# Kernel optimization log

Hardware: AMD Instinct MI355X
Metric: run time of the kernel (lower is better)

The kernel has to match this reference:

```python
import jax, jax.numpy as jnp
import numpy as np

B, S, HID = 2, 2048, 2048
H, KV, D = 16, 4, 128
ROT = 64           # partial rotary dim (= cos.shape[-1])
EMB = 128          # router embedding dim
TAU, BASE = 0.4, 3.0
EPS = 1e-6


def rotate_half(x):
    h = x.shape[-1] // 2
    return jnp.concatenate([-x[..., h:], x[..., :h]], axis=-1)


def rmsnorm(x, w, eps=EPS):
    # Qwen3.5: zero-init weight, (1 + w) scaling, compute in fp32
    xf = x.astype(jnp.float32)
    o = xf * jax.lax.rsqrt(jnp.mean(xf * xf, axis=-1, keepdims=True) + eps)
    return (o * (1.0 + w.astype(jnp.float32))).astype(x.dtype)


def _rope_tables():
    inv_freq = 1.0 / (10000.0 ** (np.arange(0, ROT, 2, dtype=np.float32) / ROT))
    t = np.arange(S, dtype=np.float32)
    freqs = np.outer(t, inv_freq)                 # [S, ROT/2]
    emb = np.concatenate([freqs, freqs], axis=-1)  # [S, ROT]
    cos = np.broadcast_to(np.cos(emb), (B, S, ROT)).copy()
    sin = np.broadcast_to(np.sin(emb), (B, S, ROT)).copy()
    return jnp.asarray(cos), jnp.asarray(sin)


def setup_inputs() -> dict:
    key = jax.random.key(0)
    ks = jax.random.split(key, 10)
    sc = 0.02
    cos, sin = _rope_tables()
    return {
        "hidden_states": jax.random.normal(ks[0], (B, S, HID), jnp.float32),
        "cos": cos,
        "sin": sin,
        # projection weights stored as [in, out] (torch Linear weight transposed)
        "Wq": jax.random.normal(ks[1], (HID, H * D * 2), jnp.float32) * sc,
        "Wk": jax.random.normal(ks[2], (HID, KV * D), jnp.float32) * sc,
        "Wv": jax.random.normal(ks[3], (HID, KV * D), jnp.float32) * sc,
        "Wo": jax.random.normal(ks[4], (H * D, HID), jnp.float32) * sc,
        "q_norm_w": jnp.zeros((D,), jnp.float32),
        "k_norm_w": jnp.zeros((D,), jnp.float32),
        "Wr": jax.random.normal(ks[5], (HID, EMB), jnp.float32) * sc,   # router linear
        "Wd": jax.random.normal(ks[6], (EMB, D), jnp.float32) * sc,     # router decoder
        "ln_g": jnp.ones((EMB,), jnp.float32),
        "ln_b": jnp.zeros((EMB,), jnp.float32),
        "rnn_state": jnp.zeros((EMB,), jnp.float32),
    }


def _forward(hidden_states, cos, sin, Wq, Wk, Wv, Wo, q_norm_w, k_norm_w,
             Wr, Wd, ln_g, ln_b, rnn_state):
    b, s, _ = hidden_states.shape
    # doubled q_proj -> query + gate
    qkv = jnp.einsum('bsh,hd->bsd', hidden_states, Wq).reshape(b, s, H, 2 * D)
    q, gate = qkv[..., :D], qkv[..., D:]
    gate = gate.reshape(b, s, H * D)
    k = jnp.einsum('bsh,hd->bsd', hidden_states, Wk).reshape(b, s, KV, D)
    v = jnp.einsum('bsh,hd->bsd', hidden_states, Wv).reshape(b, s, KV, D)
    # per-head RMSNorm then [b, h, s, d]
    q = rmsnorm(q, q_norm_w).transpose(0, 2, 1, 3)
    k = rmsnorm(k, k_norm_w).transpose(0, 2, 1, 3)
    v = v.transpose(0, 2, 1, 3)

    # --- head-dim router (gumbel-sigmoid, straight-through hard round) ---
    emb = jnp.einsum('bsh,he->bse', hidden_states, Wr) + rnn_state
    mu = jnp.mean(emb, -1, keepdims=True)
    var = jnp.mean((emb - mu) ** 2, -1, keepdims=True)
    ln = (emb - mu) * jax.lax.rsqrt(var + 1e-5) * ln_g + ln_b
    logits = jnp.einsum('bse,ed->bsd', jax.nn.gelu(ln, approximate=False), Wd)
    gum = -jnp.log(jax.random.exponential(jax.random.key(42), logits.shape, jnp.float32))
    y_soft = jax.nn.sigmoid((logits + gum + BASE) / TAU)
    binary = jax.lax.stop_gradient(jnp.round(y_soft) - y_soft) + y_soft  # [b, s, D]
    mask = binary[:, None, :, :]  # broadcast over heads: [b, 1, s, D]

    q = q * mask
    k = k * mask

    # partial RoPE on first ROT dims (qk_index=None training path)
    c = cos[:, None, :, :]
    si = sin[:, None, :, :]
    def rope(x):
        xr, xp = x[..., :ROT], x[..., ROT:]
        return jnp.concatenate([xr * c + rotate_half(xr) * si, xp], axis=-1)
    q = rope(q)
    k = rope(k)

    # GQA: repeat kv heads
    rep = H // KV
    k = jnp.repeat(k, rep, axis=1)
    v = jnp.repeat(v, rep, axis=1)

    scores = jnp.einsum('bhqd,bhkd->bhqk', q, k) / np.sqrt(D).astype(np.float32)
    causal = jnp.tril(jnp.ones((s, s), bool))
    scores = jnp.where(causal, scores, jnp.finfo(jnp.float32).min)
    attn = jax.nn.softmax(scores.astype(jnp.float32), axis=-1).astype(q.dtype)
    out = jnp.einsum('bhqk,bhkd->bhqd', attn, v)
    out = out.transpose(0, 2, 1, 3).reshape(b, s, H * D)
    out = out * jax.nn.sigmoid(gate)   # output gate
    return jnp.einsum('bsd,dh->bsh', out, Wo)


def reference(hidden_states, cos, sin, Wq, Wk, Wv, Wo, q_norm_w, k_norm_w,
              Wr, Wd, ln_g, ln_b, rnn_state):
    return _forward(hidden_states, cos, sin, Wq, Wk, Wv, Wo, q_norm_w, k_norm_w,
                    Wr, Wd, ln_g, ln_b, rnn_state)
```

## Files before the change

### kernel.cpp

```cpp
#include <hip/hip_runtime.h>
#include <math.h>

typedef __bf16 bf16;
typedef bf16 bf16x8 __attribute__((ext_vector_type(8)));
typedef bf16 bf16x4 __attribute__((ext_vector_type(4)));
typedef float f32x4 __attribute__((ext_vector_type(4)));

#define BB 2
#define SS 2048
#define HIDN 2048
#define NH 16
#define NKV 4
#define DD 128
#define NROT 64
#define NPROJ 5248

__device__ __forceinline__ float waveAllReduceSum(float v) {
#pragma unroll
  for (int o = 1; o < 64; o <<= 1) v += __shfl_xor(v, o, 64);
  return v;
}

__device__ __forceinline__ int xcd_swz(int orig, int nwg) {
  return (orig & 7) * (nwg >> 3) + (orig >> 3);
}

__device__ __forceinline__ void gload16(const bf16* g, bf16* l) {
  __builtin_amdgcn_global_load_lds((const __attribute__((address_space(1))) void*)g,
                                   (__attribute__((address_space(3))) void*)l, 16, 0, 0);
}

__device__ __forceinline__ void do_transpose(bf16 (*tile)[72], const float* __restrict__ W,
                                             bf16* __restrict__ WT, int K, int N, int rowOff,
                                             int bx, int by, int t) {
  int n0 = bx * 64, k0 = by * 64;
  {
    int c4 = (t & 15) * 4, r = t >> 4;
#pragma unroll
    for (int p = 0; p < 4; p++) {
      int row = p * 16 + r;
      float4 v = *reinterpret_cast<const float4*>(W + (size_t)(k0 + row) * N + n0 + c4);
      bf16x4 o = {(bf16)v.x, (bf16)v.y, (bf16)v.z, (bf16)v.w};
      *reinterpret_cast<bf16x4*>(&tile[row][c4]) = o;
    }
  }
  __syncthreads();
  {
    int ln = t & 7, n = t >> 3;
#pragma unroll
    for (int p = 0; p < 2; p++) {
      int nn = p * 32 + n;
      bf16x8 o;
#pragma unroll
      for (int j = 0; j < 8; j++) o[j] = tile[ln * 8 + j][nn];
      *reinterpret_cast<bf16x8*>(WT + (size_t)(rowOff + n0 + nn) * K + k0 + ln * 8) = o;
    }
  }
  __syncthreads();
}

__global__ __launch_bounds__(256) void prep_weights(const float* __restrict__ hidden,
                                                    const float* __restrict__ Wq,
                                                    const float* __restrict__ Wk,
                                                    const float* __restrict__ Wv,
                                                    const float* __restrict__ Wr,
                                                    const float* __restrict__ Wo,
                                                    bf16* __restrict__ hb,
                                                    bf16* __restrict__ WTall,
                                                    bf16* __restrict__ WoT) {
  __shared__ bf16 tile[64][72];
  int id = blockIdx.x, t = threadIdx.x;
  if (id < 4096) {
    int i = (id * 256 + t) * 8;
    float4 v0 = *reinterpret_cast<const float4*>(hidden + i);
    float4 v1 = *reinterpret_cast<const float4*>(hidden + i + 4);
    bf16x8 o = {(bf16)v0.x, (bf16)v0.y, (bf16)v0.z, (bf16)v0.w,
                (bf16)v1.x, (bf16)v1.y, (bf16)v1.z, (bf16)v1.w};
    *reinterpret_cast<bf16x8*>(hb + i) = o;
    return;
  }
  int id2 = id - 4096;
  if (id2 < 2048) { do_transpose(tile, Wq, WTall, 2048, 4096, 0, id2 & 63, id2 >> 6, t); return; }
  id2 -= 2048;
  if (id2 < 256) { do_transpose(tile, Wk, WTall, 2048, 512, 4096, id2 & 7, id2 >> 3, t); return; }
  id2 -= 256;
  if (id2 < 256) { do_transpose(tile, Wv, WTall, 2048, 512, 4608, id2 & 7, id2 >> 3, t); return; }
  id2 -= 256;
  if (id2 < 64) { do_transpose(tile, Wr, WTall, 2048, 128, 5120, id2 & 1, id2 >> 1, t); return; }
  id2 -= 64;
  do_transpose(tile, Wo, WoT, 2048, 2048, 0, id2 & 31, id2 >> 5, t);
}

template <typename CT>
__global__ __launch_bounds__(256) void gemm_bt(const bf16* __restrict__ A,
                                               const bf16* __restrict__ Bt,
                                               CT* __restrict__ C, int M, int N, int K) {
  __shared__ bf16 lA[128 * 64];
  __shared__ bf16 lB[128 * 64];
  const int nbx = N >> 7;
  int wg = xcd_swz(blockIdx.x, gridDim.x);
  int bx = wg % nbx, by = wg / nbx;
  const int t = threadIdx.x;
  const int l = t & 63, w = t >> 6;
  const int wr = w >> 1, wc = w & 1;
  const int lr = l & 15, lhi = l >> 4;

  f32x4 acc[4][4];
#pragma unroll
  for (int m = 0; m < 4; m++)
#pragma unroll
    for (int n = 0; n < 4; n++) acc[m][n] = f32x4{0.f, 0.f, 0.f, 0.f};

  const int rowA0 = by * 128, rowB0 = bx * 128;
  const int nkt = K >> 6;
  for (int kt = 0; kt < nkt; ++kt) {
    __syncthreads();
#pragma unroll
    for (int it = 0; it < 4; ++it) {
      int slot = it * 256 + t;
      int row = slot >> 3, sl = slot & 7;
      gload16(A + (size_t)(rowA0 + row) * K + kt * 64 + ((sl ^ (row & 7)) << 3), lA + slot * 8);
      gload16(Bt + (size_t)(rowB0 + row) * K + kt * 64 + ((sl ^ (row & 7)) << 3), lB + slot * 8);
    }
    __syncthreads();
#pragma unroll
    for (int kc = 0; kc < 2; ++kc) {
      bf16x8 af[4], bg[4];
#pragma unroll
      for (int m = 0; m < 4; m++) {
        int row = wr * 64 + m * 16 + lr;
        af[m] = *reinterpret_cast<const bf16x8*>((char*)lA + row * 128 + (((kc * 4 + lhi) ^ (row & 7)) << 4));
      }
#pragma unroll
      for (int n = 0; n < 4; n++) {
        int row = wc * 64 + n * 16 + lr;
        bg[n] = *reinterpret_cast<const bf16x8*>((char*)lB + row * 128 + (((kc * 4 + lhi) ^ (row & 7)) << 4));
      }
      __builtin_amdgcn_s_setprio(1);
#pragma unroll
      for (int m = 0; m < 4; m++)
#pragma unroll
        for (int n = 0; n < 4; n++)
          acc[m][n] = __builtin_amdgcn_mfma_f32_16x16x32_bf16(af[m], bg[n], acc[m][n], 0, 0, 0);
      __builtin_amdgcn_s_setprio(0);
    }
  }
#pragma unroll
  for (int m = 0; m < 4; m++)
#pragma unroll
    for (int n = 0; n < 4; n++)
#pragma unroll
      for (int r = 0; r < 4; r++) {
        int grow = rowA0 + wr * 64 + m * 16 + lhi * 4 + r;
        int gcol = rowB0 + wc * 64 + n * 16 + lr;
        C[(size_t)grow * N + gcol] = (CT)acc[m][n][r];
      }
}

__device__ __forceinline__ unsigned rotl32(unsigned x, int r) { return (x << r) | (x >> (32 - r)); }

__device__ __forceinline__ float gumbel42(unsigned i) {
  const unsigned half = (unsigned)(BB * SS * DD) / 2u;
  unsigned x0, x1;
  int word;
  if (i < half) { x0 = i; x1 = i + half; word = 0; }
  else          { x0 = i - half; x1 = i; word = 1; }
  const unsigned k0 = 0u, k1 = 42u;
  const unsigned k2 = k0 ^ k1 ^ 0x1BD11BDAu;
  x0 += k0; x1 += k1;
#define TF_R(r) { x0 += x1; x1 = rotl32(x1, r); x1 ^= x0; }
  TF_R(13) TF_R(15) TF_R(26) TF_R(6)
  x0 += k1; x1 += k2 + 1u;
  TF_R(17) TF_R(29) TF_R(16) TF_R(24)
  x0 += k2; x1 += k0 + 2u;
  TF_R(13) TF_R(15) TF_R(26) TF_R(6)
  x0 += k0; x1 += k1 + 3u;
  TF_R(17) TF_R(29) TF_R(16) TF_R(24)
  x0 += k1; x1 += k2 + 4u;
  TF_R(13) TF_R(15) TF_R(26) TF_R(6)
  x0 += k2; x1 += k0 + 5u;
#undef TF_R
  unsigned bits = word ? x1 : x0;
  float u = __uint_as_float((bits >> 9) | 0x3f800000u) - 1.0f;
  float ex = -log1pf(-u);
  return -logf(ex);
}

__global__ __launch_bounds__(128) void mask_kernel(const bf16* __restrict__ qkva,
                                                   const float* __restrict__ rnn,
                                                   const float* __restrict__ lng,
                                                   const float* __restrict__ lnb,
                                                   const float* __restrict__ Wd,
                                                   bf16* __restrict__ maskb) {
  int row = blockIdx.x;
  int t = threadIdx.x;
  int l = t & 63, w = t >> 6;
  __shared__ float redm[2], redv[2], gsh[128];
  float e = (float)qkva[(size_t)row * NPROJ + 5120 + t] + rnn[t];
  float s1 = waveAllReduceSum(e);
  if (l == 0) redm[w] = s1;
  __syncthreads();
  float mu = (redm[0] + redm[1]) * (1.0f / 128.0f);
  float dv = (e - mu) * (e - mu);
  float s2 = waveAllReduceSum(dv);
  if (l == 0) redv[w] = s2;
  __syncthreads();
  float var = (redv[0] + redv[1]) * (1.0f / 128.0f);
  float ln = (e - mu) * rsqrtf(var + 1e-5f) * lng[t] + lnb[t];
  float g = 0.5f * ln * (1.0f + erff(ln * 0.7071067811865475f));
  gsh[t] = g;
  __syncthreads();
  float logit = 0.f;
#pragma unroll 8
  for (int e2 = 0; e2 < 128; e2++) logit += gsh[e2] * Wd[e2 * 128 + t];
  float gum = gumbel42((unsigned)(row * 128 + t));
  float x = (logit + gum + 3.0f) * 2.5f;
  float y = 1.0f / (1.0f + expf(-x));
  maskb[(size_t)row * 128 + t] = (bf16)rintf(y);
}

#define QSCALE (0.08838834764831845f * 1.4426950408889634f)

__global__ __launch_bounds__(256) void qkv_prep(const bf16* __restrict__ qkva,
                                                const bf16* __restrict__ maskb,
                                                const float* __restrict__ qw,
                                                const float* __restrict__ kw,
                                                const float* __restrict__ cosT,
                                                const float* __restrict__ sinT,
                                                bf16* __restrict__ wq,
                                                bf16* __restrict__ sgate,
                                                bf16* __restrict__ wk,
                                                bf16* __restrict__ wvt) {
  int id = blockIdx.x, t = threadIdx.x;
  if (id < 4096) {
    int g = t >> 4, ln = t & 15;
    int hr = id * 16 + g;
    int h = hr & 15, row = hr >> 4;
    int b = row >> 11, s = row & 2047;
    const bf16* qp = qkva + (size_t)row * NPROJ + h * 256 + ln * 8;
    bf16x8 q8 = *reinterpret_cast<const bf16x8*>(qp);
    bf16x8 g8 = *reinterpret_cast<const bf16x8*>(qp + 128);
    bf16x8 m8 = *reinterpret_cast<const bf16x8*>(maskb + (size_t)row * 128 + ln * 8);
    float qf[8], ss = 0.f;
#pragma unroll
    for (int j = 0; j < 8; j++) { qf[j] = (float)q8[j]; ss += qf[j] * qf[j]; }
#pragma unroll
    for (int o = 1; o < 16; o <<= 1) ss += __shfl_xor(ss, o, 16);
    float rinv = rsqrtf(ss * (1.0f / 128.0f) + 1e-6f);
    alignas(16) float wv[8];
    const float4* qw4 = reinterpret_cast<const float4*>(qw);
    *reinterpret_cast<float4*>(&wv[0]) = qw4[ln * 2];
    *reinterpret_cast<float4*>(&wv[4]) = qw4[ln * 2 + 1];
    float qm[8];
#pragma unroll
    for (int j = 0; j < 8; j++) qm[j] = qf[j] * rinv * (1.0f + wv[j]) * (float)m8[j];
    alignas(16) float c8[8], s8[8];
    if (ln < 8) {
      const float4* c4 = reinterpret_cast<const float4*>(cosT + (size_t)row * 64);
      const float4* sn4 = reinterpret_cast<const float4*>(sinT + (size_t)row * 64);
      *reinterpret_cast<float4*>(&c8[0]) = c4[ln * 2];
      *reinterpret_cast<float4*>(&c8[4]) = c4[ln * 2 + 1];
      *reinterpret_cast<float4*>(&s8[0]) = sn4[ln * 2];
      *reinterpret_cast<float4*>(&s8[4]) = sn4[ln * 2 + 1];
    }
    float po[8];
#pragma unroll
    for (int j = 0; j < 8; j++) po[j] = __shfl_xor(qm[j], 4, 16);
    bf16x8 oq, og;
#pragma unroll
    for (int j = 0; j < 8; j++) {
      float ov;
      if (ln < 4) ov = qm[j] * c8[j] - po[j] * s8[j];
      else if (ln < 8) ov = qm[j] * c8[j] + po[j] * s8[j];
      else ov = qm[j];
      oq[j] = (bf16)(ov * QSCALE);
      og[j] = (bf16)(1.0f / (1.0f + expf(-(float)g8[j])));
    }
    size_t o = ((size_t)((b * 16 + h) * 2048 + s)) * 128 + ln * 8;
    *reinterpret_cast<bf16x8*>(wq + o) = oq;
    *reinterpret_cast<bf16x8*>(sgate + o) = og;
    return;
  }
  if (id < 5120) {
    int g = t >> 4, ln = t & 15;
    int hr = (id - 4096) * 16 + g;
    int kv = hr & 3, row = hr >> 2;
    int b = row >> 11, s = row & 2047;
    const bf16* kp = qkva + (size_t)row * NPROJ + 4096 + kv * 128 + ln * 8;
    bf16x8 k8 = *reinterpret_cast<const bf16x8*>(kp);
    bf16x8 m8 = *reinterpret_cast<const bf16x8*>(maskb + (size_t)row * 128 + ln * 8);
    float kf[8], ss = 0.f;
#pragma unroll
    for (int j = 0; j < 8; j++) { kf[j] = (float)k8[j]; ss += kf[j] * kf[j]; }
#pragma unroll
    for (int o = 1; o < 16; o <<= 1) ss += __shfl_xor(ss, o, 16);
    float rinv = rsqrtf(ss * (1.0f / 128.0f) + 1e-6f);
    alignas(16) float wv[8];
    const float4* kw4 = reinterpret_cast<const float4*>(kw);
    *reinterpret_cast<float4*>(&wv[0]) = kw4[ln * 2];
    *reinterpret_cast<float4*>(&wv[4]) = kw4[ln * 2 + 1];
    float km[8];
#pragma unroll
    for (int j = 0; j < 8; j++) km[j] = kf[j] * rinv * (1.0f + wv[j]) * (float)m8[j];
    alignas(16) float c8[8], s8[8];
    if (ln < 8) {
      const float4* c4 = reinterpret_cast<const float4*>(cosT + (size_t)row * 64);
      const float4* sn4 = reinterpret_cast<const float4*>(sinT + (size_t)row * 64);
      *reinterpret_cast<float4*>(&c8[0]) = c4[ln * 2];
      *reinterpret_cast<float4*>(&c8[4]) = c4[ln * 2 + 1];
      *reinterpret_cast<float4*>(&s8[0]) = sn4[ln * 2];
      *reinterpret_cast<float4*>(&s8[4]) = sn4[ln * 2 + 1];
    }
    float po[8];
#pragma unroll
    for (int j = 0; j < 8; j++) po[j] = __shfl_xor(km[j], 4, 16);
    bf16x8 ok;
#pragma unroll
    for (int j = 0; j < 8; j++) {
      float ov;
      if (ln < 4) ov = km[j] * c8[j] - po[j] * s8[j];
      else if (ln < 8) ov = km[j] * c8[j] + po[j] * s8[j];
      else ov = km[j];
      ok[j] = (bf16)ov;
    }
    *reinterpret_cast<bf16x8*>(wk + ((size_t)((b * 4 + kv) * 2048 + s)) * 128 + ln * 8) = ok;
    return;
  }
  {
    __shared__ bf16 tl[64][72];
    int vb = id - 5120;
    int dt = vb & 1;
    int st = (vb >> 1) & 31;
    int bkv = vb >> 6;
    int b = bkv >> 2, kv = bkv & 3;
    int tx = t & 63, ty = t >> 6;
    int s0 = st * 64, d0 = dt * 64;
#pragma unroll
    for (int i = 0; i < 16; i++) {
      int srow = ty + i * 4;
      tl[srow][tx] = qkva[(size_t)(b * 2048 + s0 + srow) * NPROJ + 4608 + kv * 128 + d0 + tx];
    }
    __syncthreads();
#pragma unroll
    for (int i = 0; i < 16; i++) {
      int drow = ty + i * 4;
      wvt[(size_t)((b * 4 + kv) * 128 + d0 + drow) * 2048 + s0 + tx] = tl[tx][drow];
    }
  }
}

__global__ __launch_bounds__(512) void attn_kernel(const bf16* __restrict__ wq,
                                                   const bf16* __restrict__ wk,
                                                   const bf16* __restrict__ wvt,
                                                   const bf16* __restrict__ sgate,
                                                   bf16* __restrict__ wattn) {
  __shared__ bf16 lK[2][64 * 128];
  __shared__ bf16 lV[2][128 * 64];
  __shared__ bf16 lP[8][16 * 64];
  int bid = blockIdx.x;
  int grp = bid & 7;
  int b = grp >> 2, kvh = grp & 3;
  int g32 = bid >> 3;
  int pp = g32 & 7;
  int h = kvh * 4 + (g32 >> 3);
  int bh = b * 16 + h;
  int t = threadIdx.x, l = t & 63, w = t >> 6;
  int lr = l & 15, lhi = l >> 4;

  const bf16* kbase = wk + (size_t)((b * 4 + kvh) * 2048) * 128;
  const bf16* vbase = wvt + (size_t)((b * 4 + kvh) * 128) * 2048;
  char* pb = (char*)(&lP[w][0]);

  const int n0 = 2 * pp + 2;

  auto stage = [&](int buf, int tt) {
#pragma unroll
    for (int it = 0; it < 2; ++it) {
      int slot = it * 512 + t;
      int row = slot >> 4, sl = slot & 15;
      gload16(kbase + (size_t)(tt * 64 + row) * 128 + ((sl ^ (row & 7)) << 3), lK[buf] + slot * 8);
      int row2 = slot >> 3, sl2 = slot & 7;
      gload16(vbase + (size_t)row2 * 2048 + tt * 64 + ((sl2 ^ (row2 & 7)) << 3), lV[buf] + slot * 8);
    }
  };

  bf16x8 aq[4];
  f32x4 oacc[8];
  float m_run, l_run;
  int qb128 = pp;

  auto load_q = [&](int qbv) {
    const bf16* qbase = wq + (size_t)(bh * 2048 + qbv * 128 + w * 16) * 128;
#pragma unroll
    for (int kc = 0; kc < 4; kc++)
      aq[kc] = *reinterpret_cast<const bf16x8*>(qbase + (size_t)lr * 128 + kc * 32 + lhi * 8);
  };
  load_q(pp);
#pragma unroll
  for (int db = 0; db < 8; db++) oacc[db] = f32x4{0.f, 0.f, 0.f, 0.f};
  m_run = -3.0e38f;
  l_run = 0.f;

  stage(0, 0);
  __syncthreads();
  int cur = 0;

  for (int i = 0; i < 34; ++i) {
    int tt = (i < n0) ? i : i - n0;
    if (i + 1 < 34) {
      int tn = (i + 1 < n0) ? (i + 1) : (i + 1 - n0);
      stage(cur ^ 1, tn);
    }
    int qrow0 = qb128 * 128 + w * 16;

    f32x4 sacc[4];
#pragma unroll
    for (int j = 0; j < 4; j++) sacc[j] = f32x4{0.f, 0.f, 0.f, 0.f};
    __builtin_amdgcn_s_setprio(1);
#pragma unroll
    for (int kc = 0; kc < 4; kc++)
#pragma unroll
      for (int j = 0; j < 4; j++) {
        int row = j * 16 + lr;
        bf16x8 ak = *reinterpret_cast<const bf16x8*>((char*)lK[cur] + row * 256 + (((kc * 4 + lhi) ^ (row & 7)) << 4));
        sacc[j] = __builtin_amdgcn_mfma_f32_16x16x32_bf16(ak, aq[kc], sacc[j], 0, 0, 0);
      }
    __builtin_amdgcn_s_setprio(0);

    if (tt * 64 + 63 > qrow0) {
      int qrow_g = qrow0 + lr;
#pragma unroll
      for (int j = 0; j < 4; j++)
#pragma unroll
        for (int r = 0; r < 4; r++) {
          int kg = tt * 64 + j * 16 + lhi * 4 + r;
          if (kg > qrow_g) sacc[j][r] = -1e30f;
        }
    }

    float m0 = fmaxf(fmaxf(sacc[0][0], sacc[0][1]), fmaxf(sacc[0][2], sacc[0][3]));
    float m1 = fmaxf(fmaxf(sacc[1][0], sacc[1][1]), fmaxf(sacc[1][2], sacc[1][3]));
    float m2 = fmaxf(fmaxf(sacc[2][0], sacc[2][1]), fmaxf(sacc[2][2], sacc[2][3]));
    float m3 = fmaxf(fmaxf(sacc[3][0], sacc[3][1]), fmaxf(sacc[3][2], sacc[3][3]));
    float mx = fmaxf(fmaxf(m0, m1), fmaxf(m2, m3));
    mx = fmaxf(mx, __shfl_xor(mx, 16, 64));
    mx = fmaxf(mx, __shfl_xor(mx, 32, 64));

    if (!__all(mx <= m_run + 8.0f)) {
      float mnew = fmaxf(m_run, mx);
      float corr = exp2f(m_run - mnew);
      l_run *= corr;
      m_run = mnew;
      float corr_o[4];
#pragma unroll
      for (int r = 0; r < 4; r++) corr_o[r] = __shfl(corr, lhi * 4 + r, 64);
#pragma unroll
      for (int db = 0; db < 8; db++)
#pragma unroll
        for (int r = 0; r < 4; r++) oacc[db][r] *= corr_o[r];
    }

    float p[4][4];
    float rs = 0.f;
#pragma unroll
    for (int j = 0; j < 4; j++) {
      float s0 = 0.f;
#pragma unroll
      for (int r = 0; r < 4; r++) {
        float pv = exp2f(sacc[j][r] - m_run);
        p[j][r] = pv;
        s0 += pv;
      }
      rs += s0;
    }
    rs += __shfl_xor(rs, 16, 64);
    rs += __shfl_xor(rs, 32, 64);
    l_run += rs;

#pragma unroll
    for (int j = 0; j < 4; j++) {
      bf16x4 p4 = {(bf16)p[j][0], (bf16)p[j][1], (bf16)p[j][2], (bf16)p[j][3]};
      *reinterpret_cast<bf16x4*>(pb + lr * 128 + ((j * 32 + lhi * 8) ^ ((lr & 7) << 4))) = p4;
    }
    bf16x8 pa[2];
#pragma unroll
    for (int kc2 = 0; kc2 < 2; kc2++)
      pa[kc2] = *reinterpret_cast<const bf16x8*>(pb + lr * 128 + ((kc2 * 64 + lhi * 16) ^ ((lr & 7) << 4)));
    __builtin_amdgcn_s_setprio(1);
#pragma unroll
    for (int kc2 = 0; kc2 < 2; kc2++)
#pragma unroll
      for (int db = 0; db < 8; db++) {
        int row = db * 16 + lr;
        bf16x8 bv = *reinterpret_cast<const bf16x8*>((char*)lV[cur] + row * 128 + (((kc2 * 4 + lhi) ^ (row & 7)) << 4));
        oacc[db] = __builtin_amdgcn_mfma_f32_16x16x32_bf16(pa[kc2], bv, oacc[db], 0, 0, 0);
      }
    __builtin_amdgcn_s_setprio(0);

    if (i == n0 - 1 || i == 33) {
      float linv[4];
#pragma unroll
      for (int r = 0; r < 4; r++) linv[r] = 1.0f / __shfl(l_run, lhi * 4 + r, 64);
#pragma unroll
      for (int r = 0; r < 4; r++) {
        int srow = qb128 * 128 + w * 16 + lhi * 4 + r;
#pragma unroll
        for (int db = 0; db < 8; db++) {
          int dcol = db * 16 + lr;
          float g = (float)sgate[(size_t)(bh * 2048 + srow) * 128 + dcol];
          float ov = oacc[db][r] * linv[r] * g;
          wattn[(size_t)(b * 2048 + srow) * 2048 + h * 128 + dcol] = (bf16)ov;
        }
      }
      if (i == n0 - 1) {
        qb128 = 15 - pp;
        load_q(qb128);
#pragma unroll
        for (int db = 0; db < 8; db++) oacc[db] = f32x4{0.f, 0.f, 0.f, 0.f};
        m_run = -3.0e38f;
        l_run = 0.f;
      }
    }

    __syncthreads();
    cur ^= 1;
  }
}

extern "C" void kernel_launch(void* const* d_in, const int* in_sizes, int n_in,
                              void* d_out, int out_size, void* d_ws, size_t ws_size,
                              hipStream_t stream) {
  const float* hidden = (const float*)d_in[0];
  const float* cosT = (const float*)d_in[1];
  const float* sinT = (const float*)d_in[2];
  const float* Wq = (const float*)d_in[3];
  const float* Wk = (const float*)d_in[4];
  const float* Wv = (const float*)d_in[5];
  const float* Wo = (const float*)d_in[6];
  const float* qw = (const float*)d_in[7];
  const float* kw = (const float*)d_in[8];
  const float* Wr = (const float*)d_in[9];
  const float* Wd = (const float*)d_in[10];
  const float* lng = (const float*)d_in[11];
  const float* lnb = (const float*)d_in[12];
  const float* rnn = (const float*)d_in[13];
  float* out = (float*)d_out;

  char* p = (char*)d_ws;
  auto alloc = [&](size_t bytes) { char* r = p; p += (bytes + 255) & ~(size_t)255; return r; };
  bf16* hb    = (bf16*)alloc((size_t)4096 * 2048 * 2);
  bf16* WTall = (bf16*)alloc((size_t)NPROJ * 2048 * 2);
  bf16* WoT   = (bf16*)alloc((size_t)2048 * 2048 * 2);
  bf16* qkva  = (bf16*)alloc((size_t)4096 * NPROJ * 2);
  bf16* maskb = (bf16*)alloc((size_t)4096 * 128 * 2);
  bf16* wqb   = (bf16*)alloc((size_t)2 * 16 * 2048 * 128 * 2);
  bf16* wkb   = (bf16*)alloc((size_t)2 * 4 * 2048 * 128 * 2);
  bf16* wvtb  = (bf16*)alloc((size_t)2 * 4 * 128 * 2048 * 2);
  bf16* sgb   = (bf16*)alloc((size_t)2 * 16 * 2048 * 128 * 2);
  bf16* wab   = (bf16*)alloc((size_t)4096 * 2048 * 2);
  if ((size_t)(p - (char*)d_ws) > ws_size) return;

  prep_weights<<<7744, 256, 0, stream>>>(hidden, Wq, Wk, Wv, Wr, Wo, hb, WTall, WoT);

  gemm_bt<bf16><<<41 * 32, 256, 0, stream>>>(hb, WTall, qkva, 4096, NPROJ, 2048);

  mask_kernel<<<4096, 128, 0, stream>>>(qkva, rnn, lng, lnb, Wd, maskb);
  qkv_prep<<<5632, 256, 0, stream>>>(qkva, maskb, qw, kw, cosT, sinT, wqb, sgb, wkb, wvtb);

  attn_kernel<<<256, 512, 0, stream>>>(wqb, wkb, wvtb, sgb, wab);

  gemm_bt<float><<<16 * 32, 256, 0, stream>>>(wab, WoT, out, 4096, 2048, 2048);
}
```

Before: 279.1 us.

## Fuse QKV projection GEMM with norm, RoPE, mask, gate and V transpose epilogue

The router embedding columns are split into a small separate GEMM so the mask can be computed first. The main QKV GEMM then applies RMSNorm, masking, partial RoPE, sigmoid gating and the V transpose directly from LDS in its epilogue. This drops the round trip of the large qkva intermediate through global memory and removes the separate prep kernel. In exchange, the 32-block router GEMM is a small serialized launch that uses the GPU poorly, and the epilogue adds LDS traffic and branching inside the GEMM kernel.

```diff
diff --git a/kernel.cpp b/kernel.cpp
--- a/kernel.cpp
+++ b/kernel.cpp
@@ -8,12 +8,8 @@
 
 #define BB 2
 #define SS 2048
-#define HIDN 2048
-#define NH 16
-#define NKV 4
-#define DD 128
-#define NROT 64
-#define NPROJ 5248
+#define NPROJ 5120
+#define QSCALE (0.08838834764831845f * 1.4426950408889634f)
 
 __device__ __forceinline__ float waveAllReduceSum(float v) {
 #pragma unroll
@@ -157,10 +153,187 @@
       }
 }
 
+#define EPL 136
+__global__ __launch_bounds__(256) void proj_fused(const bf16* __restrict__ A,
+                                                  const bf16* __restrict__ Bt,
+                                                  const bf16* __restrict__ maskb,
+                                                  const float* __restrict__ qw,
+                                                  const float* __restrict__ kw,
+                                                  const float* __restrict__ cosT,
+                                                  const float* __restrict__ sinT,
+                                                  bf16* __restrict__ wq,
+                                                  bf16* __restrict__ sgate,
+                                                  bf16* __restrict__ wk,
+                                                  bf16* __restrict__ wvt) {
+  __shared__ bf16 smem[128 * EPL];
+  bf16* lA = smem;
+  bf16* lB = smem + 128 * 64;
+  const int nbx = 40;
+  int wg = xcd_swz(blockIdx.x, gridDim.x);
+  int bx = wg % nbx, by = wg / nbx;
+  const int t = threadIdx.x;
+  const int l = t & 63, w = t >> 6;
+  const int wr = w >> 1, wc = w & 1;
+  const int lr = l & 15, lhi = l >> 4;
+  const int K = 2048;
+
+  f32x4 acc[4][4];
+#pragma unroll
+  for (int m = 0; m < 4; m++)
+#pragma unroll
+    for (int n = 0; n < 4; n++) acc[m][n] = f32x4{0.f, 0.f, 0.f, 0.f};
+
+  const int rowA0 = by * 128, rowB0 = bx * 128;
+  for (int kt = 0; kt < 32; ++kt) {
+    __syncthreads();
+#pragma unroll
+    for (int it = 0; it < 4; ++it) {
+      int slot = it * 256 + t;
+      int row = slot >> 3, sl = slot & 7;
+      gload16(A + (size_t)(rowA0 + row) * K + kt * 64 + ((sl ^ (row & 7)) << 3), lA + slot * 8);
+      gload16(Bt + (size_t)(rowB0 + row) * K + kt * 64 + ((sl ^ (row & 7)) << 3), lB + slot * 8);
+    }
+    __syncthreads();
+#pragma unroll
+    for (int kc = 0; kc < 2; ++kc) {
+      bf16x8 af[4], bg[4];
+#pragma unroll
+      for (int m = 0; m < 4; m++) {
+        int row = wr * 64 + m * 16 + lr;
+        af[m] = *reinterpret_cast<const bf16x8*>((char*)lA + row * 128 + (((kc * 4 + lhi) ^ (row & 7)) << 4));
+      }
+#pragma unroll
+      for (int n = 0; n < 4; n++) {
+        int row = wc * 64 + n * 16 + lr;
+        bg[n] = *reinterpret_cast<const bf16x8*>((char*)lB + row * 128 + (((kc * 4 + lhi) ^ (row & 7)) << 4));
+      }
+      __builtin_amdgcn_s_setprio(1);
+#pragma unroll
+      for (int m = 0; m < 4; m++)
+#pragma unroll
+        for (int n = 0; n < 4; n++)
+          acc[m][n] = __builtin_amdgcn_mfma_f32_16x16x32_bf16(af[m], bg[n], acc[m][n], 0, 0, 0);
+      __builtin_amdgcn_s_setprio(0);
+    }
+  }
+
+  __syncthreads();
+#pragma unroll
+  for (int m = 0; m < 4; m++)
+#pragma unroll
+    for (int n = 0; n < 4; n++)
+#pragma unroll
+      for (int r = 0; r < 4; r++)
+        smem[(wr * 64 + m * 16 + lhi * 4 + r) * EPL + wc * 64 + n * 16 + lr] = (bf16)acc[m][n][r];
+  __syncthreads();
+
+  const int cx = bx;
+  const int b = rowA0 >> 11;
+  const int s0 = rowA0 & 2047;
+
+  if (cx >= 36) {
+    int kv = cx - 36;
+    int d = t >> 1, shalf = (t & 1) * 64;
+    bf16* dst = wvt + ((size_t)((b * 4 + kv) * 128 + d)) * 2048 + s0 + shalf;
+#pragma unroll
+    for (int sc = 0; sc < 8; sc++) {
+      bf16x8 col;
+#pragma unroll
+      for (int j = 0; j < 8; j++) col[j] = smem[(shalf + sc * 8 + j) * EPL + d];
+      *reinterpret_cast<bf16x8*>(dst + sc * 8) = col;
+    }
+    return;
+  }
+
+  int rr = t >> 1, half = t & 1, d0 = half * 64;
+  int sg = s0 + rr;
+  const bf16* eprow = smem + rr * EPL + d0;
+
+  if (cx < 32 && (cx & 1)) {
+    int h = cx >> 1;
+    bf16* dst = sgate + ((size_t)(b * 16 + h) * 2048 + sg) * 128 + d0;
+#pragma unroll
+    for (int c = 0; c < 8; c++) {
+      bf16x8 v = *reinterpret_cast<const bf16x8*>(eprow + c * 8);
+      bf16x8 o;
+#pragma unroll
+      for (int j = 0; j < 8; j++) o[j] = (bf16)(1.0f / (1.0f + expf(-(float)v[j])));
+      *reinterpret_cast<bf16x8*>(dst + c * 8) = o;
+    }
+    return;
+  }
+
+  bool isq = cx < 32;
+  const float* nw = isq ? qw : kw;
+  float ss = 0.f;
+#pragma unroll
+  for (int c = 0; c < 8; c++) {
+    bf16x8 v = *reinterpret_cast<const bf16x8*>(eprow + c * 8);
+#pragma unroll
+    for (int j = 0; j < 8; j++) { float f = (float)v[j]; ss += f * f; }
+  }
+  ss += __shfl_xor(ss, 1, 64);
+  float rinv = rsqrtf(ss * (1.0f / 128.0f) + 1e-6f);
+  const bf16* mrow = maskb + (size_t)(rowA0 + rr) * 128 + d0;
+  bf16* dst;
+  float oscale;
+  if (isq) {
+    int h = cx >> 1;
+    dst = wq + ((size_t)(b * 16 + h) * 2048 + sg) * 128 + d0;
+    oscale = QSCALE;
+  } else {
+    int kv = cx - 32;
+    dst = wk + ((size_t)(b * 4 + kv) * 2048 + sg) * 128 + d0;
+    oscale = 1.0f;
+  }
+  if (half == 0) {
+    const float* crow = cosT + (size_t)(rowA0 + rr) * 64;
+    const float* srow = sinT + (size_t)(rowA0 + rr) * 64;
+#pragma unroll
+    for (int c = 0; c < 4; c++) {
+      bf16x8 va = *reinterpret_cast<const bf16x8*>(eprow + c * 8);
+      bf16x8 vb = *reinterpret_cast<const bf16x8*>(eprow + c * 8 + 32);
+      bf16x8 ma = *reinterpret_cast<const bf16x8*>(mrow + c * 8);
+      bf16x8 mb = *reinterpret_cast<const bf16x8*>(mrow + c * 8 + 32);
+      float qa[8], qb[8];
+#pragma unroll
+      for (int j = 0; j < 8; j++) {
+        int d = c * 8 + j;
+        qa[j] = (float)va[j] * rinv * (1.0f + nw[d]) * (float)ma[j];
+        qb[j] = (float)vb[j] * rinv * (1.0f + nw[d + 32]) * (float)mb[j];
+      }
+      bf16x8 oa, ob;
+#pragma unroll
+      for (int j = 0; j < 8; j++) {
+        int d = c * 8 + j;
+        float outa = qa[j] * crow[d] - qb[j] * srow[d];
+        float outb = qb[j] * crow[d + 32] + qa[j] * srow[d + 32];
+        oa[j] = (bf16)(outa * oscale);
+        ob[j] = (bf16)(outb * oscale);
+      }
+      *reinterpret_cast<bf16x8*>(dst + c * 8) = oa;
+      *reinterpret_cast<bf16x8*>(dst + c * 8 + 32) = ob;
+    }
+  } else {
+#pragma unroll
+    for (int c = 0; c < 8; c++) {
+      bf16x8 v = *reinterpret_cast<const bf16x8*>(eprow + c * 8);
+      bf16x8 m8 = *reinterpret_cast<const bf16x8*>(mrow + c * 8);
+      bf16x8 o;
+#pragma unroll
+      for (int j = 0; j < 8; j++) {
+        int d = d0 + c * 8 + j;
+        o[j] = (bf16)((float)v[j] * rinv * (1.0f + nw[d]) * (float)m8[j] * oscale);
+      }
+      *reinterpret_cast<bf16x8*>(dst + c * 8) = o;
+    }
+  }
+}
+
 __device__ __forceinline__ unsigned rotl32(unsigned x, int r) { return (x << r) | (x >> (32 - r)); }
 
 __device__ __forceinline__ float gumbel42(unsigned i) {
-  const unsigned half = (unsigned)(BB * SS * DD) / 2u;
+  const unsigned half = (unsigned)(BB * SS * 128) / 2u;
   unsigned x0, x1;
   int word;
   if (i < half) { x0 = i; x1 = i + half; word = 0; }
@@ -186,7 +359,7 @@
   return -logf(ex);
 }
 
-__global__ __launch_bounds__(128) void mask_kernel(const bf16* __restrict__ qkva,
+__global__ __launch_bounds__(128) void mask_kernel(const bf16* __restrict__ embb,
                                                    const float* __restrict__ rnn,
                                                    const float* __restrict__ lng,
                                                    const float* __restrict__ lnb,
@@ -196,7 +369,7 @@
   int t = threadIdx.x;
   int l = t & 63, w = t >> 6;
   __shared__ float redm[2], redv[2], gsh[128];
-  float e = (float)qkva[(size_t)row * NPROJ + 5120 + t] + rnn[t];
+  float e = (float)embb[(size_t)row * 128 + t] + rnn[t];
   float s1 = waveAllReduceSum(e);
   if (l == 0) redm[w] = s1;
   __syncthreads();
@@ -217,136 +390,6 @@
   float x = (logit + gum + 3.0f) * 2.5f;
   float y = 1.0f / (1.0f + expf(-x));
   maskb[(size_t)row * 128 + t] = (bf16)rintf(y);
-}
-
-#define QSCALE (0.08838834764831845f * 1.4426950408889634f)
-
-__global__ __launch_bounds__(256) void qkv_prep(const bf16* __restrict__ qkva,
-                                                const bf16* __restrict__ maskb,
-                                                const float* __restrict__ qw,
-                                                const float* __restrict__ kw,
-                                                const float* __restrict__ cosT,
-                                                const float* __restrict__ sinT,
-                                                bf16* __restrict__ wq,
-                                                bf16* __restrict__ sgate,
-                                                bf16* __restrict__ wk,
-                                                bf16* __restrict__ wvt) {
-  int id = blockIdx.x, t = threadIdx.x;
-  if (id < 4096) {
-    int g = t >> 4, ln = t & 15;
-    int hr = id * 16 + g;
-    int h = hr & 15, row = hr >> 4;
-    int b = row >> 11, s = row & 2047;
-    const bf16* qp = qkva + (size_t)row * NPROJ + h * 256 + ln * 8;
-    bf16x8 q8 = *reinterpret_cast<const bf16x8*>(qp);
-    bf16x8 g8 = *reinterpret_cast<const bf16x8*>(qp + 128);
-    bf16x8 m8 = *reinterpret_cast<const bf16x8*>(maskb + (size_t)row * 128 + ln * 8);
-    float qf[8], ss = 0.f;
-#pragma unroll
-    for (int j = 0; j < 8; j++) { qf[j] = (float)q8[j]; ss += qf[j] * qf[j]; }
-#pragma unroll
-    for (int o = 1; o < 16; o <<= 1) ss += __shfl_xor(ss, o, 16);
-    float rinv = rsqrtf(ss * (1.0f / 128.0f) + 1e-6f);
-    alignas(16) float wv[8];
-    const float4* qw4 = reinterpret_cast<const float4*>(qw);
-    *reinterpret_cast<float4*>(&wv[0]) = qw4[ln * 2];
-    *reinterpret_cast<float4*>(&wv[4]) = qw4[ln * 2 + 1];
-    float qm[8];
-#pragma unroll
-    for (int j = 0; j < 8; j++) qm[j] = qf[j] * rinv * (1.0f + wv[j]) * (float)m8[j];
-    alignas(16) float c8[8], s8[8];
-    if (ln < 8) {
-      const float4* c4 = reinterpret_cast<const float4*>(cosT + (size_t)row * 64);
-      const float4* sn4 = reinterpret_cast<const float4*>(sinT + (size_t)row * 64);
-      *reinterpret_cast<float4*>(&c8[0]) = c4[ln * 2];
-      *reinterpret_cast<float4*>(&c8[4]) = c4[ln * 2 + 1];
-      *reinterpret_cast<float4*>(&s8[0]) = sn4[ln * 2];
-      *reinterpret_cast<float4*>(&s8[4]) = sn4[ln * 2 + 1];
-    }
-    float po[8];
-#pragma unroll
-    for (int j = 0; j < 8; j++) po[j] = __shfl_xor(qm[j], 4, 16);
-    bf16x8 oq, og;
-#pragma unroll
-    for (int j = 0; j < 8; j++) {
-      float ov;
-      if (ln < 4) ov = qm[j] * c8[j] - po[j] * s8[j];
-      else if (ln < 8) ov = qm[j] * c8[j] + po[j] * s8[j];
-      else ov = qm[j];
-      oq[j] = (bf16)(ov * QSCALE);
-      og[j] = (bf16)(1.0f / (1.0f + expf(-(float)g8[j])));
-    }
-    size_t o = ((size_t)((b * 16 + h) * 2048 + s)) * 128 + ln * 8;
-    *reinterpret_cast<bf16x8*>(wq + o) = oq;
-    *reinterpret_cast<bf16x8*>(sgate + o) = og;
-    return;
-  }
-  if (id < 5120) {
-    int g = t >> 4, ln = t & 15;
-    int hr = (id - 4096) * 16 + g;
-    int kv = hr & 3, row = hr >> 2;
-    int b = row >> 11, s = row & 2047;
-    const bf16* kp = qkva + (size_t)row * NPROJ + 4096 + kv * 128 + ln * 8;
-    bf16x8 k8 = *reinterpret_cast<const bf16x8*>(kp);
-    bf16x8 m8 = *reinterpret_cast<const bf16x8*>(maskb + (size_t)row * 128 + ln * 8);
-    float kf[8], ss = 0.f;
-#pragma unroll
-    for (int j = 0; j < 8; j++) { kf[j] = (float)k8[j]; ss += kf[j] * kf[j]; }
-#pragma unroll
-    for (int o = 1; o < 16; o <<= 1) ss += __shfl_xor(ss, o, 16);
-    float rinv = rsqrtf(ss * (1.0f / 128.0f) + 1e-6f);
-    alignas(16) float wv[8];
-    const float4* kw4 = reinterpret_cast<const float4*>(kw);
-    *reinterpret_cast<float4*>(&wv[0]) = kw4[ln * 2];
-    *reinterpret_cast<float4*>(&wv[4]) = kw4[ln * 2 + 1];
-    float km[8];
-#pragma unroll
-    for (int j = 0; j < 8; j++) km[j] = kf[j] * rinv * (1.0f + wv[j]) * (float)m8[j];
-    alignas(16) float c8[8], s8[8];
-    if (ln < 8) {
-      const float4* c4 = reinterpret_cast<const float4*>(cosT + (size_t)row * 64);
-      const float4* sn4 = reinterpret_cast<const float4*>(sinT + (size_t)row * 64);
-      *reinterpret_cast<float4*>(&c8[0]) = c4[ln * 2];
-      *reinterpret_cast<float4*>(&c8[4]) = c4[ln * 2 + 1];
-      *reinterpret_cast<float4*>(&s8[0]) = sn4[ln * 2];
-      *reinterpret_cast<float4*>(&s8[4]) = sn4[ln * 2 + 1];
-    }
-    float po[8];
-#pragma unroll
-    for (int j = 0; j < 8; j++) po[j] = __shfl_xor(km[j], 4, 16);
-    bf16x8 ok;
-#pragma unroll
-    for (int j = 0; j < 8; j++) {
-      float ov;
-      if (ln < 4) ov = km[j] * c8[j] - po[j] * s8[j];
-      else if (ln < 8) ov = km[j] * c8[j] + po[j] * s8[j];
-      else ov = km[j];
-      ok[j] = (bf16)ov;
-    }
-    *reinterpret_cast<bf16x8*>(wk + ((size_t)((b * 4 + kv) * 2048 + s)) * 128 + ln * 8) = ok;
-    return;
-  }
-  {
-    __shared__ bf16 tl[64][72];
-    int vb = id - 5120;
-    int dt = vb & 1;
-    int st = (vb >> 1) & 31;
-    int bkv = vb >> 6;
-    int b = bkv >> 2, kv = bkv & 3;
-    int tx = t & 63, ty = t >> 6;
-    int s0 = st * 64, d0 = dt * 64;
-#pragma unroll
-    for (int i = 0; i < 16; i++) {
-      int srow = ty + i * 4;
-      tl[srow][tx] = qkva[(size_t)(b * 2048 + s0 + srow) * NPROJ + 4608 + kv * 128 + d0 + tx];
-    }
-    __syncthreads();
-#pragma unroll
-    for (int i = 0; i < 16; i++) {
-      int drow = ty + i * 4;
-      wvt[(size_t)((b * 4 + kv) * 128 + d0 + drow) * 2048 + s0 + tx] = tl[tx][drow];
-    }
-  }
 }
 
 __global__ __launch_bounds__(512) void attn_kernel(const bf16* __restrict__ wq,
@@ -549,9 +592,9 @@
   char* p = (char*)d_ws;
   auto alloc = [&](size_t bytes) { char* r = p; p += (bytes + 255) & ~(size_t)255; return r; };
   bf16* hb    = (bf16*)alloc((size_t)4096 * 2048 * 2);
-  bf16* WTall = (bf16*)alloc((size_t)NPROJ * 2048 * 2);
+  bf16* WTall = (bf16*)alloc((size_t)5248 * 2048 * 2);
   bf16* WoT   = (bf16*)alloc((size_t)2048 * 2048 * 2);
-  bf16* qkva  = (bf16*)alloc((size_t)4096 * NPROJ * 2);
+  bf16* embb  = (bf16*)alloc((size_t)4096 * 128 * 2);
   bf16* maskb = (bf16*)alloc((size_t)4096 * 128 * 2);
   bf16* wqb   = (bf16*)alloc((size_t)2 * 16 * 2048 * 128 * 2);
   bf16* wkb   = (bf16*)alloc((size_t)2 * 4 * 2048 * 128 * 2);
@@ -562,10 +605,11 @@
 
   prep_weights<<<7744, 256, 0, stream>>>(hidden, Wq, Wk, Wv, Wr, Wo, hb, WTall, WoT);
 
-  gemm_bt<bf16><<<41 * 32, 256, 0, stream>>>(hb, WTall, qkva, 4096, NPROJ, 2048);
-
-  mask_kernel<<<4096, 128, 0, stream>>>(qkva, rnn, lng, lnb, Wd, maskb);
-  qkv_prep<<<5632, 256, 0, stream>>>(qkva, maskb, qw, kw, cosT, sinT, wqb, sgb, wkb, wvtb);
+  gemm_bt<bf16><<<32, 256, 0, stream>>>(hb, WTall + (size_t)5120 * 2048, embb, 4096, 128, 2048);
+
+  mask_kernel<<<4096, 128, 0, stream>>>(embb, rnn, lng, lnb, Wd, maskb);
+
+  proj_fused<<<1280, 256, 0, stream>>>(hb, WTall, maskb, qw, kw, cosT, sinT, wqb, sgb, wkb, wvtb);
 
   attn_kernel<<<256, 512, 0, stream>>>(wqb, wkb, wvtb, sgb, wab);
 
```

Result: slower. 320.4 us (+14.8%).
